# Optimization experiments

Hardware: AMD Instinct MI355X
Metric: run time of the kernel (lower is better)

Reference implementation:

```python
import jax, jax.numpy as jnp
import numpy as np

N_NODES = 50000
N_EDGES = 640000
F_IN = 64
EDGE_DIM = 16
HID = 128
N_LAYERS = 3
N_CLASSES = 2
NUM_GRAPHS = 64
BN_EPS = 1e-5


def setup_inputs() -> dict:
    key = jax.random.key(0)
    ks = jax.random.split(key, 20)
    s = 0.05
    inp = {
        "x": jax.random.normal(ks[0], (N_NODES, F_IN), dtype=jnp.float32),
        "edge_index": jax.random.randint(ks[1], (2, N_EDGES), 0, N_NODES, dtype=jnp.int32),
        "edge_attr": jax.random.normal(ks[2], (N_EDGES, EDGE_DIM), dtype=jnp.float32),
        "batch": jnp.sort(jax.random.randint(ks[3], (N_NODES,), 0, NUM_GRAPHS, dtype=jnp.int32)),
        # node encoder
        "enc_W": jax.random.normal(ks[4], (F_IN, HID), dtype=jnp.float32) * s,
        "enc_b": jnp.zeros((HID,), dtype=jnp.float32),
        # per-layer GINEConv params (stacked over layers)
        "edge_W": jax.random.normal(ks[5], (N_LAYERS, EDGE_DIM, HID), dtype=jnp.float32) * s,
        "edge_b": jnp.zeros((N_LAYERS, HID), dtype=jnp.float32),
        "mlp_W1": jax.random.normal(ks[6], (N_LAYERS, HID, HID), dtype=jnp.float32) * s,
        "mlp_b1": jnp.zeros((N_LAYERS, HID), dtype=jnp.float32),
        "mlp_W2": jax.random.normal(ks[7], (N_LAYERS, HID, HID), dtype=jnp.float32) * s,
        "mlp_b2": jnp.zeros((N_LAYERS, HID), dtype=jnp.float32),
        "bn_gamma": jnp.ones((N_LAYERS, HID), dtype=jnp.float32),
        "bn_beta": jnp.zeros((N_LAYERS, HID), dtype=jnp.float32),
        # classification head
        "head_W1": jax.random.normal(ks[8], (HID, HID), dtype=jnp.float32) * s,
        "head_b1": jnp.zeros((HID,), dtype=jnp.float32),
        "head_W2": jax.random.normal(ks[9], (HID, N_CLASSES), dtype=jnp.float32) * s,
        "head_b2": jnp.zeros((N_CLASSES,), dtype=jnp.float32),
    }
    return inp


def reference(x, edge_index, edge_attr, batch, enc_W, enc_b, edge_W, edge_b,
              mlp_W1, mlp_b1, mlp_W2, mlp_b2, bn_gamma, bn_beta,
              head_W1, head_b1, head_W2, head_b2):
    src, dst = edge_index[0], edge_index[1]  # message flows src -> dst
    h = x @ enc_W + enc_b  # [N, HID]
    for l in range(N_LAYERS):
        # GINEConv: msg = ReLU(x_src + Lin(edge_attr)); aggr = scatter_add at dst
        e = edge_attr @ edge_W[l] + edge_b[l]          # [E, HID]
        msg = jax.nn.relu(h[src] + e)                  # [E, HID]
        agg = jax.ops.segment_sum(msg, dst, num_segments=N_NODES)
        z = h + agg  # (1 + eps) * x + aggr, eps = 0
        # node MLP: Linear-ReLU-Linear
        z = jax.nn.relu(z @ mlp_W1[l] + mlp_b1[l]) @ mlp_W2[l] + mlp_b2[l]
        # BatchNorm1d (training-mode batch stats) + ReLU (dropout = identity)
        mean = jnp.mean(z, axis=0)
        var = jnp.var(z, axis=0)
        z = bn_gamma[l] * (z - mean) * jax.lax.rsqrt(var + BN_EPS) + bn_beta[l]
        h = jax.nn.relu(z)
    # global_add_pool over graphs
    g = jax.ops.segment_sum(h, batch, num_segments=NUM_GRAPHS)  # [G, HID]
    out = jax.nn.relu(g @ head_W1 + head_b1) @ head_W2 + head_b2
    return out  # [G, N_CLASSES]
```

## Files before the change

### kernel.cpp

```cpp
#include <hip/hip_runtime.h>
#include <hip/hip_bf16.h>

#define N_NODES 50000
#define N_EDGES 640000
#define F_IN 64
#define EDGE_DIM 16
#define HID 128
#define N_LAYERS 3
#define NUM_GRAPHS 64
#define BN_EPS 1e-5f

typedef __attribute__((ext_vector_type(8))) short short8;
typedef __attribute__((ext_vector_type(4))) float f32x4;
typedef __attribute__((ext_vector_type(2))) __fp16 half2v;

__device__ __forceinline__ float bfl(unsigned int u) {
    unsigned int v = u << 16; float f; __builtin_memcpy(&f, &v, 4); return f;
}
__device__ __forceinline__ float bfh(unsigned int u) {
    unsigned int v = u & 0xffff0000u; float f; __builtin_memcpy(&f, &v, 4); return f;
}
__device__ __forceinline__ unsigned int f2bf(float f) {
    unsigned int v; __builtin_memcpy(&v, &f, 4);
    v += 0x7fffu + ((v >> 16) & 1u);
    return v >> 16;
}
__device__ __forceinline__ unsigned int pack2(float lo, float hi) {
    return f2bf(lo) | (f2bf(hi) << 16);
}
__device__ __forceinline__ half2v u2h(unsigned int u) {
    half2v h; __builtin_memcpy(&h, &u, 4); return h;
}
__device__ __forceinline__ unsigned int pkh(float a, float b) {
    half2v h = __builtin_amdgcn_cvt_pkrtz(a, b);
    unsigned int u; __builtin_memcpy(&u, &h, 4); return u;
}

__global__ void k_hist(const int* __restrict__ dst, int* __restrict__ deg) {
    int e = blockIdx.x * 256 + threadIdx.x;
    atomicAdd(&deg[dst[e]], 1);
}

__global__ void k_blockred(const int* __restrict__ deg, int* __restrict__ bsums) {
    __shared__ int s[256];
    int i = blockIdx.x * 256 + threadIdx.x;
    int v = (i < N_NODES) ? deg[i] : 0;
    s[threadIdx.x] = v;
    __syncthreads();
    for (int off = 128; off > 0; off >>= 1) {
        if (threadIdx.x < off) s[threadIdx.x] += s[threadIdx.x + off];
        __syncthreads();
    }
    if (threadIdx.x == 0) bsums[blockIdx.x] = s[0];
}

__global__ void k_scan_bsums(int* __restrict__ bsums, int nb) {
    if (threadIdx.x == 0) {
        int run = 0;
        for (int i = 0; i < nb; ++i) { int v = bsums[i]; bsums[i] = run; run += v; }
    }
}

__global__ void k_scan_blocks(int* __restrict__ deg_rowptr, const int* __restrict__ bsums,
                              int* __restrict__ cursor) {
    __shared__ int s[256];
    int tid = threadIdx.x;
    int i = blockIdx.x * 256 + tid;
    int v = (i < N_NODES) ? deg_rowptr[i] : 0;
    s[tid] = v;
    __syncthreads();
    for (int off = 1; off < 256; off <<= 1) {
        int t = 0;
        if (tid >= off) t = s[tid - off];
        __syncthreads();
        s[tid] += t;
        __syncthreads();
    }
    int excl = s[tid] - v + bsums[blockIdx.x];
    if (i < N_NODES) {
        deg_rowptr[i] = excl;
        cursor[i] = excl;
    }
    if (i == N_NODES - 1) deg_rowptr[N_NODES] = N_EDGES;
}

__global__ void k_fill(const int* __restrict__ dst, int* __restrict__ cursor,
                       int* __restrict__ elist) {
    int e = blockIdx.x * 256 + threadIdx.x;
    int p = atomicAdd(&cursor[dst[e]], 1);
    elist[p] = e;
}

__global__ void k_gather(const int* __restrict__ elist, const int* __restrict__ esrc,
                         const float* __restrict__ eattr,
                         int* __restrict__ src_s, uint4* __restrict__ eattr_h) {
    const int p = blockIdx.x * 256 + threadIdx.x;
    const int eid = elist[p];
    src_s[p] = esrc[eid];
    const float4 a0 = *(const float4*)&eattr[eid * EDGE_DIM];
    const float4 a1 = *(const float4*)&eattr[eid * EDGE_DIM + 4];
    const float4 a2 = *(const float4*)&eattr[eid * EDGE_DIM + 8];
    const float4 a3 = *(const float4*)&eattr[eid * EDGE_DIM + 12];
    eattr_h[p * 2] = make_uint4(pkh(a0.x, a0.y), pkh(a0.z, a0.w),
                                pkh(a1.x, a1.y), pkh(a1.z, a1.w));
    eattr_h[p * 2 + 1] = make_uint4(pkh(a2.x, a2.y), pkh(a2.z, a2.w),
                                    pkh(a3.x, a3.y), pkh(a3.z, a3.w));
}

__global__ void k_packW(const float* __restrict__ W1, const float* __restrict__ W2,
                        unsigned short* __restrict__ wp) {
    const int t = blockIdx.x * 256 + threadIdx.x;
    const int mat = t >> 11;
    const int r = t & 2047;
    const int kstep = r >> 9;
    const int ntile = (r >> 6) & 7;
    const int lane = r & 63;
    const float* W = (mat < 3) ? (W1 + mat * 16384) : (W2 + (mat - 3) * 16384);
    const int kbase = kstep * 32 + ((lane >> 4) << 3);
    const int n = ntile * 16 + (lane & 15);
    unsigned int o[4];
#pragma unroll
    for (int jj = 0; jj < 4; ++jj)
        o[jj] = pack2(W[(kbase + 2 * jj) * HID + n], W[(kbase + 2 * jj + 1) * HID + n]);
    *(uint4*)(wp + (size_t)mat * 16384 + (((kstep << 3) + ntile) * 64 + lane) * 8) =
        make_uint4(o[0], o[1], o[2], o[3]);
}

__global__ void k_packEnc(const float* __restrict__ W, unsigned short* __restrict__ wpe) {
    const int t = blockIdx.x * 256 + threadIdx.x;
    const int kstep = t >> 9;
    const int ntile = (t >> 6) & 7;
    const int lane = t & 63;
    const int kbase = kstep * 32 + ((lane >> 4) << 3);
    const int n = ntile * 16 + (lane & 15);
    unsigned int o[4];
#pragma unroll
    for (int jj = 0; jj < 4; ++jj)
        o[jj] = pack2(W[(kbase + 2 * jj) * HID + n], W[(kbase + 2 * jj + 1) * HID + n]);
    *(uint4*)(wpe + (((kstep << 3) + ntile) * 64 + lane) * 8) =
        make_uint4(o[0], o[1], o[2], o[3]);
}

__global__ void k_packWe(const float* __restrict__ eW, unsigned int* __restrict__ wek) {
    const int t = blockIdx.x * 256 + threadIdx.x;
    const int l = t >> 10;
    const int r = t & 1023;
    const int kp = r >> 7, f = r & 127;
    const float a = eW[(l * EDGE_DIM + 2 * kp) * HID + f];
    const float b = eW[(l * EDGE_DIM + 2 * kp + 1) * HID + f];
    wek[t] = pkh(a, b);
}

__global__ void k_xcast(const float* __restrict__ x, unsigned int* __restrict__ xb32) {
    const int i = blockIdx.x * 256 + threadIdx.x;
    const float2 v = *(const float2*)&x[i * 2];
    xb32[i] = pack2(v.x, v.y);
}

__global__ __launch_bounds__(256, 3) void k_encm(const unsigned short* __restrict__ xb,
                                                 const unsigned short* __restrict__ wpe,
                                                 const float* __restrict__ b,
                                                 unsigned short* __restrict__ hb) {
    const int tid = threadIdx.x;
    const int w = tid >> 6, lane = tid & 63;
    const int q = lane >> 4, l15 = lane & 15;
    const int row0 = blockIdx.x * 64 + w * 16;
    const int ar = min(row0 + l15, N_NODES - 1);
    const unsigned short* aptr = xb + (size_t)ar * F_IN + q * 8;
    f32x4 acc[8];
#pragma unroll
    for (int nt = 0; nt < 8; ++nt) acc[nt] = (f32x4){0.f, 0.f, 0.f, 0.f};
#pragma unroll
    for (int ks = 0; ks < 2; ++ks) {
        const short8 a = *(const short8*)(aptr + ks * 32);
#pragma unroll
        for (int nt = 0; nt < 8; ++nt) {
            const short8 bf = *(const short8*)(wpe + (((ks << 3) + nt) * 64 + lane) * 8);
            acc[nt] = __builtin_amdgcn_mfma_f32_16x16x32_bf16(a, bf, acc[nt], 0, 0, 0);
        }
    }
    const int rowb = row0 + q * 4;
#pragma unroll
    for (int nt = 0; nt < 8; ++nt) {
        const float bias = b[nt * 16 + l15];
        const int cc = nt * 16 + l15;
#pragma unroll
        for (int reg = 0; reg < 4; ++reg) {
            const int r = rowb + reg;
            if (r < N_NODES)
                hb[(size_t)r * HID + cc] = (unsigned short)f2bf(acc[nt][reg] + bias);
        }
    }
}

__global__ __launch_bounds__(256, 2) void k_agg(const unsigned int* __restrict__ hb32,
                                                const int* __restrict__ src_s,
                                                const uint4* __restrict__ eattr_h,
                                                const unsigned int* __restrict__ wek,
                                                const float* __restrict__ be,
                                                const int* __restrict__ row_ptr,
                                                unsigned int* __restrict__ zb32) {
    const int lane = threadIdx.x & 63;
    const int wv = threadIdx.x >> 6;
    const int f2 = lane * 2;
    half2v wx[8], wy[8];
#pragma unroll
    for (int j = 0; j < 8; ++j) {
        wx[j] = u2h(wek[j * 128 + f2]);
        wy[j] = u2h(wek[j * 128 + f2 + 1]);
    }
    const float2 eb = *(const float2*)&be[f2];

    const int n = blockIdx.x * 4 + wv;
    const int base = __builtin_amdgcn_readfirstlane(row_ptr[n]);
    const int deg = __builtin_amdgcn_readfirstlane(row_ptr[n + 1]) - base;

    const unsigned int hself = hb32[n * 64 + lane];
    float2 acc = make_float2(bfl(hself), bfh(hself));

    if (deg > 0) {
        const int* sp = src_s + base;
        const uint4* ep = eattr_h + (size_t)base * 2;
        const int last = deg - 1;
        const int nch = (deg + 3) >> 2;

        unsigned int huC[4], huN[4];
        uint4 eaC[4][2], eaN[4][2];
        int s2[4];
        {
            int s0[4], s1[4];
#pragma unroll
            for (int j = 0; j < 4; ++j) s0[j] = sp[min(j, last)];
#pragma unroll
            for (int j = 0; j < 4; ++j) huC[j] = hb32[s0[j] * 64 + lane];
#pragma unroll
            for (int j = 0; j < 4; ++j) s1[j] = sp[min(4 + j, last)];
            if (nch > 1) {
#pragma unroll
                for (int j = 0; j < 4; ++j) huN[j] = hb32[s1[j] * 64 + lane];
            } else {
#pragma unroll
                for (int j = 0; j < 4; ++j) huN[j] = 0u;
            }
#pragma unroll
            for (int j = 0; j < 4; ++j) {
                const int e = min(j, last);
                eaC[j][0] = ep[e * 2]; eaC[j][1] = ep[e * 2 + 1];
            }
#pragma unroll
            for (int j = 0; j < 4; ++j) s2[j] = sp[min(8 + j, last)];
        }
        for (int c = 0; c < nch; ++c) {
            unsigned int huNN[4] = {0u, 0u, 0u, 0u};
            if (c + 2 < nch) {
#pragma unroll
                for (int j = 0; j < 4; ++j) huNN[j] = hb32[s2[j] * 64 + lane];
            }
            int s3[4];
#pragma unroll
            for (int j = 0; j < 4; ++j) s3[j] = sp[min((c + 3) * 4 + j, last)];
            if (c + 1 < nch) {
#pragma unroll
                for (int j = 0; j < 4; ++j) {
                    const int e = min((c + 1) * 4 + j, last);
                    eaN[j][0] = ep[e * 2]; eaN[j][1] = ep[e * 2 + 1];
                }
            }
            const int rem = deg - c * 4;
#pragma unroll
            for (int j = 0; j < 4; ++j) {
                if (j < rem) {
                    const unsigned int* au = (const unsigned int*)&eaC[j][0];
                    float ex = eb.x, ey = eb.y;
#pragma unroll
                    for (int k = 0; k < 8; ++k) {
                        const half2v a = u2h(au[k]);
                        ex = __builtin_amdgcn_fdot2(a, wx[k], ex, false);
                        ey = __builtin_amdgcn_fdot2(a, wy[k], ey, false);
                    }
                    acc.x += fmaxf(bfl(huC[j]) + ex, 0.f);
                    acc.y += fmaxf(bfh(huC[j]) + ey, 0.f);
                }
            }
            if (c + 1 < nch) {
#pragma unroll
                for (int j = 0; j < 4; ++j) {
                    huC[j] = huN[j]; huN[j] = huNN[j];
                    eaC[j][0] = eaN[j][0]; eaC[j][1] = eaN[j][1];
                    s2[j] = s3[j];
                }
            }
        }
    }
    zb32[n * 64 + lane] = pack2(acc.x, acc.y);
}

#define Z1LD 136

__global__ __launch_bounds__(256, 3) void k_mlp(const unsigned short* __restrict__ zb,
                                                const unsigned short* __restrict__ w1p,
                                                const float* __restrict__ b1,
                                                const unsigned short* __restrict__ w2p,
                                                const float* __restrict__ b2,
                                                unsigned short* __restrict__ z2b,
                                                float* __restrict__ bn) {
    __shared__ unsigned short z1s[64 * Z1LD];
    __shared__ float redA[512];
    __shared__ float redB[512];
    const int tid = threadIdx.x;
    const int w = tid >> 6, lane = tid & 63;
    const int q = lane >> 4, l15 = lane & 15;
    const int row0 = blockIdx.x * 64 + w * 16;

    const int ar = min(row0 + l15, N_NODES - 1);
    const unsigned short* aptr = zb + (size_t)ar * HID + q * 8;

    f32x4 acc[8];
#pragma unroll
    for (int nt = 0; nt < 8; ++nt) acc[nt] = (f32x4){0.f, 0.f, 0.f, 0.f};

#pragma unroll
    for (int ks = 0; ks < 4; ++ks) {
        const short8 a = *(const short8*)(aptr + ks * 32);
#pragma unroll
        for (int nt = 0; nt < 8; ++nt) {
            const short8 b = *(const short8*)(w1p + (((ks << 3) + nt) * 64 + lane) * 8);
            acc[nt] = __builtin_amdgcn_mfma_f32_16x16x32_bf16(a, b, acc[nt], 0, 0, 0);
        }
    }
    {
        const int lr0 = w * 16 + q * 4;
#pragma unroll
        for (int nt = 0; nt < 8; ++nt) {
            const float bias = b1[nt * 16 + l15];
            const int cc = nt * 16 + l15;
#pragma unroll
            for (int reg = 0; reg < 4; ++reg) {
                const float v = fmaxf(acc[nt][reg] + bias, 0.f);
                z1s[(lr0 + reg) * Z1LD + cc] = (unsigned short)f2bf(v);
            }
        }
    }
#pragma unroll
    for (int nt = 0; nt < 8; ++nt) acc[nt] = (f32x4){0.f, 0.f, 0.f, 0.f};
    const unsigned short* a2p = &z1s[(w * 16 + l15) * Z1LD + q * 8];
#pragma unroll
    for (int ks = 0; ks < 4; ++ks) {
        const short8 a = *(const short8*)(a2p + ks * 32);
#pragma unroll
        for (int nt = 0; nt < 8; ++nt) {
            const short8 b = *(const short8*)(w2p + (((ks << 3) + nt) * 64 + lane) * 8);
            acc[nt] = __builtin_amdgcn_mfma_f32_16x16x32_bf16(a, b, acc[nt], 0, 0, 0);
        }
    }
    float s[8], sq[8];
    const int rowb = row0 + q * 4;
#pragma unroll
    for (int nt = 0; nt < 8; ++nt) {
        const float bias = b2[nt * 16 + l15];
        const int cc = nt * 16 + l15;
        float ls = 0.f, lq = 0.f;
#pragma unroll
        for (int reg = 0; reg < 4; ++reg) {
            const int r = rowb + reg;
            const float v = acc[nt][reg] + bias;
            if (r < N_NODES) {
                z2b[(size_t)r * HID + cc] = (unsigned short)f2bf(v);
                ls += v;
                lq = fmaf(v, v, lq);
            }
        }
        s[nt] = ls; sq[nt] = lq;
    }
#pragma unroll
    for (int nt = 0; nt < 8; ++nt) {
        s[nt] += __shfl_xor(s[nt], 16, 64);
        s[nt] += __shfl_xor(s[nt], 32, 64);
        sq[nt] += __shfl_xor(sq[nt], 16, 64);
        sq[nt] += __shfl_xor(sq[nt], 32, 64);
    }
    if (lane < 16) {
#pragma unroll
        for (int nt = 0; nt < 8; ++nt) {
            redA[w * 128 + nt * 16 + lane] = s[nt];
            redB[w * 128 + nt * 16 + lane] = sq[nt];
        }
    }
    __syncthreads();
    if (tid < 128) {
        float t = redA[tid] + redA[128 + tid] + redA[256 + tid] + redA[384 + tid];
        atomicAdd(&bn[tid], t);
    } else {
        const int c = tid - 128;
        float t = redB[c] + redB[128 + c] + redB[256 + c] + redB[384 + c];
        atomicAdd(&bn[128 + c], t);
    }
}

__global__ __launch_bounds__(256) void k_bnrelu(const unsigned short* __restrict__ z2b,
                                                const float* __restrict__ bn,
                                                const float* __restrict__ gamma,
                                                const float* __restrict__ beta,
                                                unsigned short* __restrict__ hb) {
    const int idx = (blockIdx.x * 256 + threadIdx.x) * 4;
    const int c = idx & 127;
    const float invN = 1.0f / (float)N_NODES;
    const uint2 zz = *(const uint2*)(z2b + idx);
    float o[4] = {bfl(zz.x), bfh(zz.x), bfl(zz.y), bfh(zz.y)};
#pragma unroll
    for (int k = 0; k < 4; ++k) {
        const float m = bn[c + k] * invN;
        float var = bn[128 + c + k] * invN - m * m;
        var = fmaxf(var, 0.f);
        const float r = rsqrtf(var + BN_EPS);
        o[k] = fmaxf(gamma[c + k] * (o[k] - m) * r + beta[c + k], 0.f);
    }
    *(uint2*)&hb[idx] = make_uint2(pack2(o[0], o[1]), pack2(o[2], o[3]));
}

__global__ void k_pool(const unsigned short* __restrict__ hb, const int* __restrict__ batch,
                       float* __restrict__ g) {
    const int f = threadIdx.x;
    const int n0 = blockIdx.x * 128;
    const int nend = min(n0 + 128, N_NODES);
    float acc = 0.f;
    int cur = batch[n0];
    for (int n = n0; n < nend; ++n) {
        const int bb = batch[n];
        if (bb != cur) {
            atomicAdd(&g[cur * HID + f], acc);
            acc = 0.f;
            cur = bb;
        }
        acc += bfl((unsigned int)hb[n * HID + f]);
    }
    atomicAdd(&g[cur * HID + f], acc);
}

__global__ void k_head1(const float* __restrict__ g, const float* __restrict__ W,
                        const float* __restrict__ b, float* __restrict__ g1) {
    const int idx = blockIdx.x * 256 + threadIdx.x;
    const int r = idx >> 7, c = idx & 127;
    float acc = b[c];
    for (int k = 0; k < 128; ++k) acc = fmaf(g[r * HID + k], W[k * HID + c], acc);
    g1[idx] = fmaxf(acc, 0.f);
}

__global__ void k_head2(const float* __restrict__ g1, const float* __restrict__ W,
                        const float* __restrict__ b, float* __restrict__ out) {
    const int idx = threadIdx.x;
    const int r = idx >> 1, c = idx & 1;
    float acc = b[c];
    for (int k = 0; k < 128; ++k) acc = fmaf(g1[r * HID + k], W[k * 2 + c], acc);
    out[idx] = acc;
}

extern "C" void kernel_launch(void* const* d_in, const int* in_sizes, int n_in,
                              void* d_out, int out_size, void* d_ws, size_t ws_size,
                              hipStream_t stream) {
    const float* x     = (const float*)d_in[0];
    const int*   ei    = (const int*)d_in[1];
    const float* eattr = (const float*)d_in[2];
    const int*   batch = (const int*)d_in[3];
    const float* encW  = (const float*)d_in[4];
    const float* encb  = (const float*)d_in[5];
    const float* eW    = (const float*)d_in[6];
    const float* eb    = (const float*)d_in[7];
    const float* W1    = (const float*)d_in[8];
    const float* b1    = (const float*)d_in[9];
    const float* W2    = (const float*)d_in[10];
    const float* b2    = (const float*)d_in[11];
    const float* gam   = (const float*)d_in[12];
    const float* bet   = (const float*)d_in[13];
    const float* hW1   = (const float*)d_in[14];
    const float* hb1   = (const float*)d_in[15];
    const float* hW2   = (const float*)d_in[16];
    const float* hb2   = (const float*)d_in[17];
    float* out = (float*)d_out;

    float* ws = (float*)d_ws;
    unsigned short* z2b = (unsigned short*)ws;
    float* bn  = ws + 3200000;
    float* g   = ws + 3200256;
    float* g1  = ws + 3208448;
    unsigned short* hb = (unsigned short*)(ws + 3216640);
    unsigned int* zb32 = (unsigned int*)(ws + 6416640);
    unsigned int* xb32 = (unsigned int*)(ws + 9616640);
    int* row_ptr = (int*)(ws + 11216640);
    int* cursor  = row_ptr + N_NODES + 1;
    int* elist   = cursor + N_NODES;
    int* bsums   = elist + N_EDGES;
    int* src_s   = bsums + 256;
    uint4* eattr_h = (uint4*)(ws + 12596900);
    unsigned short* wp  = (unsigned short*)(ws + 17716900);
    unsigned short* wpe = (unsigned short*)(ws + 17766100);
    unsigned int*   wek = (unsigned int*)(ws + 17770200);

    const int* esrc = ei;
    const int* edst = ei + N_EDGES;

    hipMemsetAsync(row_ptr, 0, (N_NODES + 1) * sizeof(int), stream);
    k_hist<<<N_EDGES / 256, 256, 0, stream>>>(edst, row_ptr);
    k_blockred<<<196, 256, 0, stream>>>(row_ptr, bsums);
    k_scan_bsums<<<1, 64, 0, stream>>>(bsums, 196);
    k_scan_blocks<<<196, 256, 0, stream>>>(row_ptr, bsums, cursor);
    k_fill<<<N_EDGES / 256, 256, 0, stream>>>(edst, cursor, elist);
    k_gather<<<N_EDGES / 256, 256, 0, stream>>>(elist, esrc, eattr, src_s, eattr_h);

    k_packW<<<48, 256, 0, stream>>>(W1, W2, wp);
    k_packEnc<<<4, 256, 0, stream>>>(encW, wpe);
    k_packWe<<<12, 256, 0, stream>>>(eW, wek);

    k_xcast<<<6250, 256, 0, stream>>>(x, xb32);
    k_encm<<<782, 256, 0, stream>>>((const unsigned short*)xb32, wpe, encb, hb);

    for (int l = 0; l < N_LAYERS; ++l) {
        k_agg<<<12500, 256, 0, stream>>>((const unsigned int*)hb, src_s, eattr_h,
                                         wek + l * 1024, eb + l * HID, row_ptr, zb32);
        hipMemsetAsync(bn, 0, 256 * sizeof(float), stream);
        k_mlp<<<782, 256, 0, stream>>>((const unsigned short*)zb32,
                                       wp + (size_t)l * 16384, b1 + l * HID,
                                       wp + (size_t)(3 + l) * 16384, b2 + l * HID,
                                       z2b, bn);
        k_bnrelu<<<6250, 256, 0, stream>>>(z2b, bn, gam + l * HID, bet + l * HID, hb);
    }

    hipMemsetAsync(g, 0, NUM_GRAPHS * HID * sizeof(float), stream);
    k_pool<<<391, 128, 0, stream>>>(hb, batch, g);
    k_head1<<<32, 256, 0, stream>>>(g, hW1, hb1, g1);
    k_head2<<<1, 128, 0, stream>>>(g1, hW2, hb2, out);
}
```

Measured before the change: 609.3 us.

## Merge pack kernels, fuse x cast into encoder, persistent aggregation grid

Combines the three weight-packing kernels into one launch and folds the fp32-to-bf16 cast of x into the encoder MFMA kernel, which removes launches and an intermediate buffer round trip. The serial single-thread bsums scan becomes a parallel shared-memory scan. k_gather now handles four edges per thread to expose more memory-level parallelism. k_agg switches to a grid-stride persistent grid of 2048 blocks, so each wave processes many nodes and the weights it loads into registers are reused across them, at some risk of load imbalance across waves.

Result: no change. 608.9 us (-0.1%).

```diff
diff --git a/kernel.cpp b/kernel.cpp
--- a/kernel.cpp
+++ b/kernel.cpp
@@ -9,6 +9,9 @@
 #define N_LAYERS 3
 #define NUM_GRAPHS 64
 #define BN_EPS 1e-5f
+
+#define AGG_BLOCKS 2048
+#define AGG_WAVES (AGG_BLOCKS * 4)
 
 typedef __attribute__((ext_vector_type(8))) short short8;
 typedef __attribute__((ext_vector_type(4))) float f32x4;
@@ -55,10 +58,19 @@
 }
 
 __global__ void k_scan_bsums(int* __restrict__ bsums, int nb) {
-    if (threadIdx.x == 0) {
-        int run = 0;
-        for (int i = 0; i < nb; ++i) { int v = bsums[i]; bsums[i] = run; run += v; }
-    }
+    __shared__ int s[256];
+    const int tid = threadIdx.x;
+    const int v = (tid < nb) ? bsums[tid] : 0;
+    s[tid] = v;
+    __syncthreads();
+    for (int off = 1; off < 256; off <<= 1) {
+        int t = 0;
+        if (tid >= off) t = s[tid - off];
+        __syncthreads();
+        s[tid] += t;
+        __syncthreads();
+    }
+    if (tid < nb) bsums[tid] = s[tid] - v;
 }
 
 __global__ void k_scan_blocks(int* __restrict__ deg_rowptr, const int* __restrict__ bsums,
@@ -91,73 +103,85 @@
     elist[p] = e;
 }
 
-__global__ void k_gather(const int* __restrict__ elist, const int* __restrict__ esrc,
-                         const float* __restrict__ eattr,
-                         int* __restrict__ src_s, uint4* __restrict__ eattr_h) {
-    const int p = blockIdx.x * 256 + threadIdx.x;
-    const int eid = elist[p];
-    src_s[p] = esrc[eid];
-    const float4 a0 = *(const float4*)&eattr[eid * EDGE_DIM];
-    const float4 a1 = *(const float4*)&eattr[eid * EDGE_DIM + 4];
-    const float4 a2 = *(const float4*)&eattr[eid * EDGE_DIM + 8];
-    const float4 a3 = *(const float4*)&eattr[eid * EDGE_DIM + 12];
-    eattr_h[p * 2] = make_uint4(pkh(a0.x, a0.y), pkh(a0.z, a0.w),
-                                pkh(a1.x, a1.y), pkh(a1.z, a1.w));
-    eattr_h[p * 2 + 1] = make_uint4(pkh(a2.x, a2.y), pkh(a2.z, a2.w),
-                                    pkh(a3.x, a3.y), pkh(a3.z, a3.w));
-}
-
-__global__ void k_packW(const float* __restrict__ W1, const float* __restrict__ W2,
-                        unsigned short* __restrict__ wp) {
+__global__ __launch_bounds__(256) void k_gather(const int* __restrict__ elist,
+                                                const int* __restrict__ esrc,
+                                                const float* __restrict__ eattr,
+                                                int* __restrict__ src_s,
+                                                uint4* __restrict__ eattr_h) {
+    const int base = blockIdx.x * 1024;
+    const int tid = threadIdx.x;
+    int p[4], eid[4];
+#pragma unroll
+    for (int j = 0; j < 4; ++j) p[j] = base + tid + j * 256;
+#pragma unroll
+    for (int j = 0; j < 4; ++j) eid[j] = elist[p[j]];
+    int sv[4];
+#pragma unroll
+    for (int j = 0; j < 4; ++j) sv[j] = esrc[eid[j]];
+    float4 a[4][4];
+#pragma unroll
+    for (int j = 0; j < 4; ++j) {
+        const float* ep = eattr + (size_t)eid[j] * EDGE_DIM;
+        a[j][0] = *(const float4*)ep;
+        a[j][1] = *(const float4*)(ep + 4);
+        a[j][2] = *(const float4*)(ep + 8);
+        a[j][3] = *(const float4*)(ep + 12);
+    }
+#pragma unroll
+    for (int j = 0; j < 4; ++j) {
+        src_s[p[j]] = sv[j];
+        eattr_h[p[j] * 2] = make_uint4(pkh(a[j][0].x, a[j][0].y), pkh(a[j][0].z, a[j][0].w),
+                                       pkh(a[j][1].x, a[j][1].y), pkh(a[j][1].z, a[j][1].w));
+        eattr_h[p[j] * 2 + 1] = make_uint4(pkh(a[j][2].x, a[j][2].y), pkh(a[j][2].z, a[j][2].w),
+                                           pkh(a[j][3].x, a[j][3].y), pkh(a[j][3].z, a[j][3].w));
+    }
+}
+
+__global__ void k_pack(const float* __restrict__ W1, const float* __restrict__ W2,
+                       const float* __restrict__ encW, const float* __restrict__ eW,
+                       unsigned short* __restrict__ wp, unsigned short* __restrict__ wpe,
+                       unsigned int* __restrict__ wek) {
     const int t = blockIdx.x * 256 + threadIdx.x;
-    const int mat = t >> 11;
-    const int r = t & 2047;
-    const int kstep = r >> 9;
-    const int ntile = (r >> 6) & 7;
-    const int lane = r & 63;
-    const float* W = (mat < 3) ? (W1 + mat * 16384) : (W2 + (mat - 3) * 16384);
-    const int kbase = kstep * 32 + ((lane >> 4) << 3);
-    const int n = ntile * 16 + (lane & 15);
-    unsigned int o[4];
-#pragma unroll
-    for (int jj = 0; jj < 4; ++jj)
-        o[jj] = pack2(W[(kbase + 2 * jj) * HID + n], W[(kbase + 2 * jj + 1) * HID + n]);
-    *(uint4*)(wp + (size_t)mat * 16384 + (((kstep << 3) + ntile) * 64 + lane) * 8) =
-        make_uint4(o[0], o[1], o[2], o[3]);
-}
-
-__global__ void k_packEnc(const float* __restrict__ W, unsigned short* __restrict__ wpe) {
-    const int t = blockIdx.x * 256 + threadIdx.x;
-    const int kstep = t >> 9;
-    const int ntile = (t >> 6) & 7;
-    const int lane = t & 63;
-    const int kbase = kstep * 32 + ((lane >> 4) << 3);
-    const int n = ntile * 16 + (lane & 15);
-    unsigned int o[4];
-#pragma unroll
-    for (int jj = 0; jj < 4; ++jj)
-        o[jj] = pack2(W[(kbase + 2 * jj) * HID + n], W[(kbase + 2 * jj + 1) * HID + n]);
-    *(uint4*)(wpe + (((kstep << 3) + ntile) * 64 + lane) * 8) =
-        make_uint4(o[0], o[1], o[2], o[3]);
-}
-
-__global__ void k_packWe(const float* __restrict__ eW, unsigned int* __restrict__ wek) {
-    const int t = blockIdx.x * 256 + threadIdx.x;
-    const int l = t >> 10;
-    const int r = t & 1023;
-    const int kp = r >> 7, f = r & 127;
-    const float a = eW[(l * EDGE_DIM + 2 * kp) * HID + f];
-    const float b = eW[(l * EDGE_DIM + 2 * kp + 1) * HID + f];
-    wek[t] = pkh(a, b);
-}
-
-__global__ void k_xcast(const float* __restrict__ x, unsigned int* __restrict__ xb32) {
-    const int i = blockIdx.x * 256 + threadIdx.x;
-    const float2 v = *(const float2*)&x[i * 2];
-    xb32[i] = pack2(v.x, v.y);
-}
-
-__global__ __launch_bounds__(256, 3) void k_encm(const unsigned short* __restrict__ xb,
+    if (t < 12288) {
+        const int mat = t >> 11;
+        const int r = t & 2047;
+        const int kstep = r >> 9;
+        const int ntile = (r >> 6) & 7;
+        const int lane = r & 63;
+        const float* W = (mat < 3) ? (W1 + mat * 16384) : (W2 + (mat - 3) * 16384);
+        const int kbase = kstep * 32 + ((lane >> 4) << 3);
+        const int n = ntile * 16 + (lane & 15);
+        unsigned int o[4];
+#pragma unroll
+        for (int jj = 0; jj < 4; ++jj)
+            o[jj] = pack2(W[(kbase + 2 * jj) * HID + n], W[(kbase + 2 * jj + 1) * HID + n]);
+        *(uint4*)(wp + (size_t)mat * 16384 + (((kstep << 3) + ntile) * 64 + lane) * 8) =
+            make_uint4(o[0], o[1], o[2], o[3]);
+    } else if (t < 13312) {
+        const int r = t - 12288;
+        const int kstep = r >> 9;
+        const int ntile = (r >> 6) & 7;
+        const int lane = r & 63;
+        const int kbase = kstep * 32 + ((lane >> 4) << 3);
+        const int n = ntile * 16 + (lane & 15);
+        unsigned int o[4];
+#pragma unroll
+        for (int jj = 0; jj < 4; ++jj)
+            o[jj] = pack2(encW[(kbase + 2 * jj) * HID + n], encW[(kbase + 2 * jj + 1) * HID + n]);
+        *(uint4*)(wpe + (((kstep << 3) + ntile) * 64 + lane) * 8) =
+            make_uint4(o[0], o[1], o[2], o[3]);
+    } else {
+        const int r = t - 13312;
+        const int l = r >> 10;
+        const int rr = r & 1023;
+        const int kp = rr >> 7, f = rr & 127;
+        const float a = eW[(l * EDGE_DIM + 2 * kp) * HID + f];
+        const float b = eW[(l * EDGE_DIM + 2 * kp + 1) * HID + f];
+        wek[r] = pkh(a, b);
+    }
+}
+
+__global__ __launch_bounds__(256, 3) void k_encm(const float* __restrict__ x,
                                                  const unsigned short* __restrict__ wpe,
                                                  const float* __restrict__ b,
                                                  unsigned short* __restrict__ hb) {
@@ -166,13 +190,17 @@
     const int q = lane >> 4, l15 = lane & 15;
     const int row0 = blockIdx.x * 64 + w * 16;
     const int ar = min(row0 + l15, N_NODES - 1);
-    const unsigned short* aptr = xb + (size_t)ar * F_IN + q * 8;
+    const float* xp = x + (size_t)ar * F_IN + q * 8;
     f32x4 acc[8];
 #pragma unroll
     for (int nt = 0; nt < 8; ++nt) acc[nt] = (f32x4){0.f, 0.f, 0.f, 0.f};
 #pragma unroll
     for (int ks = 0; ks < 2; ++ks) {
-        const short8 a = *(const short8*)(aptr + ks * 32);
+        const float4 v0 = *(const float4*)(xp + ks * 32);
+        const float4 v1 = *(const float4*)(xp + ks * 32 + 4);
+        unsigned int u[4] = {pack2(v0.x, v0.y), pack2(v0.z, v0.w),
+                             pack2(v1.x, v1.y), pack2(v1.z, v1.w)};
+        short8 a; __builtin_memcpy(&a, u, 16);
 #pragma unroll
         for (int nt = 0; nt < 8; ++nt) {
             const short8 bf = *(const short8*)(wpe + (((ks << 3) + nt) * 64 + lane) * 8);
@@ -210,89 +238,91 @@
         wy[j] = u2h(wek[j * 128 + f2 + 1]);
     }
     const float2 eb = *(const float2*)&be[f2];
-
-    const int n = blockIdx.x * 4 + wv;
-    const int base = __builtin_amdgcn_readfirstlane(row_ptr[n]);
-    const int deg = __builtin_amdgcn_readfirstlane(row_ptr[n + 1]) - base;
-
-    const unsigned int hself = hb32[n * 64 + lane];
-    float2 acc = make_float2(bfl(hself), bfh(hself));
-
-    if (deg > 0) {
-        const int* sp = src_s + base;
-        const uint4* ep = eattr_h + (size_t)base * 2;
-        const int last = deg - 1;
-        const int nch = (deg + 3) >> 2;
-
-        unsigned int huC[4], huN[4];
-        uint4 eaC[4][2], eaN[4][2];
-        int s2[4];
-        {
-            int s0[4], s1[4];
-#pragma unroll
-            for (int j = 0; j < 4; ++j) s0[j] = sp[min(j, last)];
-#pragma unroll
-            for (int j = 0; j < 4; ++j) huC[j] = hb32[s0[j] * 64 + lane];
-#pragma unroll
-            for (int j = 0; j < 4; ++j) s1[j] = sp[min(4 + j, last)];
-            if (nch > 1) {
-#pragma unroll
-                for (int j = 0; j < 4; ++j) huN[j] = hb32[s1[j] * 64 + lane];
-            } else {
-#pragma unroll
-                for (int j = 0; j < 4; ++j) huN[j] = 0u;
+    const int wgid = blockIdx.x * 4 + wv;
+
+    for (int n = wgid; n < N_NODES; n += AGG_WAVES) {
+        const int base = __builtin_amdgcn_readfirstlane(row_ptr[n]);
+        const int deg = __builtin_amdgcn_readfirstlane(row_ptr[n + 1]) - base;
+
+        const unsigned int hself = hb32[n * 64 + lane];
+        float2 acc = make_float2(bfl(hself), bfh(hself));
+
+        if (deg > 0) {
+            const int* sp = src_s + base;
+            const uint4* ep = eattr_h + (size_t)base * 2;
+            const int last = deg - 1;
+            const int nch = (deg + 3) >> 2;
+
+            unsigned int huC[4], huN[4];
+            uint4 eaC[4][2], eaN[4][2];
+            int s2[4];
+            {
+                int s0[4], s1[4];
+#pragma unroll
+                for (int j = 0; j < 4; ++j) s0[j] = sp[min(j, last)];
+#pragma unroll
+                for (int j = 0; j < 4; ++j) huC[j] = hb32[s0[j] * 64 + lane];
+#pragma unroll
+                for (int j = 0; j < 4; ++j) s1[j] = sp[min(4 + j, last)];
+                if (nch > 1) {
+#pragma unroll
+                    for (int j = 0; j < 4; ++j) huN[j] = hb32[s1[j] * 64 + lane];
+                } else {
+#pragma unroll
+                    for (int j = 0; j < 4; ++j) huN[j] = 0u;
+                }
+#pragma unroll
+                for (int j = 0; j < 4; ++j) {
+                    const int e = min(j, last);
+                    eaC[j][0] = ep[e * 2]; eaC[j][1] = ep[e * 2 + 1];
+                }
+#pragma unroll
+                for (int j = 0; j < 4; ++j) s2[j] = sp[min(8 + j, last)];
             }
-#pragma unroll
-            for (int j = 0; j < 4; ++j) {
-                const int e = min(j, last);
-                eaC[j][0] = ep[e * 2]; eaC[j][1] = ep[e * 2 + 1];
-            }
-#pragma unroll
-            for (int j = 0; j < 4; ++j) s2[j] = sp[min(8 + j, last)];
-        }
-        for (int c = 0; c < nch; ++c) {
-            unsigned int huNN[4] = {0u, 0u, 0u, 0u};
-            if (c + 2 < nch) {
-#pragma unroll
-                for (int j = 0; j < 4; ++j) huNN[j] = hb32[s2[j] * 64 + lane];
-            }
-            int s3[4];
-#pragma unroll
-            for (int j = 0; j < 4; ++j) s3[j] = sp[min((c + 3) * 4 + j, last)];
-            if (c + 1 < nch) {
+            for (int c = 0; c < nch; ++c) {
+                unsigned int huNN[4] = {0u, 0u, 0u, 0u};
+                if (c + 2 < nch) {
+#pragma unroll
+                    for (int j = 0; j < 4; ++j) huNN[j] = hb32[s2[j] * 64 + lane];
+                }
+                int s3[4];
+#pragma unroll
+                for (int j = 0; j < 4; ++j) s3[j] = sp[min((c + 3) * 4 + j, last)];
+                if (c + 1 < nch) {
+#pragma unroll
+                    for (int j = 0; j < 4; ++j) {
+                        const int e = min((c + 1) * 4 + j, last);
+                        eaN[j][0] = ep[e * 2]; eaN[j][1] = ep[e * 2 + 1];
+                    }
+                }
+                const int rem = deg - c * 4;
 #pragma unroll
                 for (int j = 0; j < 4; ++j) {
-                    const int e = min((c + 1) * 4 + j, last);
-                    eaN[j][0] = ep[e * 2]; eaN[j][1] = ep[e * 2 + 1];
+                    if (j < rem) {
+                        const unsigned int* au = (const unsigned int*)&eaC[j][0];
+                        float ex = eb.x, ey = eb.y;
+#pragma unroll
+                        for (int k = 0; k < 8; ++k) {
+                            const half2v a = u2h(au[k]);
+                            ex = __builtin_amdgcn_fdot2(a, wx[k], ex, false);
+                            ey = __builtin_amdgcn_fdot2(a, wy[k], ey, false);
+                        }
+                        acc.x += fmaxf(bfl(huC[j]) + ex, 0.f);
+                        acc.y += fmaxf(bfh(huC[j]) + ey, 0.f);
+                    }
+                }
+                if (c + 1 < nch) {
+#pragma unroll
+                    for (int j = 0; j < 4; ++j) {
+                        huC[j] = huN[j]; huN[j] = huNN[j];
+                        eaC[j][0] = eaN[j][0]; eaC[j][1] = eaN[j][1];
+                        s2[j] = s3[j];
+                    }
                 }
             }
-            const int rem = deg - c * 4;
-#pragma unroll
-            for (int j = 0; j < 4; ++j) {
-                if (j < rem) {
-                    const unsigned int* au = (const unsigned int*)&eaC[j][0];
-                    float ex = eb.x, ey = eb.y;
-#pragma unroll
-                    for (int k = 0; k < 8; ++k) {
-                        const half2v a = u2h(au[k]);
-                        ex = __builtin_amdgcn_fdot2(a, wx[k], ex, false);
-                        ey = __builtin_amdgcn_fdot2(a, wy[k], ey, false);
-                    }
-                    acc.x += fmaxf(bfl(huC[j]) + ex, 0.f);
-                    acc.y += fmaxf(bfh(huC[j]) + ey, 0.f);
-                }
-            }
-            if (c + 1 < nch) {
-#pragma unroll
-                for (int j = 0; j < 4; ++j) {
-                    huC[j] = huN[j]; huN[j] = huNN[j];
-                    eaC[j][0] = eaN[j][0]; eaC[j][1] = eaN[j][1];
-                    s2[j] = s3[j];
-                }
-            }
-        }
-    }
-    zb32[n * 64 + lane] = pack2(acc.x, acc.y);
+        }
+        zb32[n * 64 + lane] = pack2(acc.x, acc.y);
+    }
 }
 
 #define Z1LD 136
@@ -485,7 +515,6 @@
     float* g1  = ws + 3208448;
     unsigned short* hb = (unsigned short*)(ws + 3216640);
     unsigned int* zb32 = (unsigned int*)(ws + 6416640);
-    unsigned int* xb32 = (unsigned int*)(ws + 9616640);
     int* row_ptr = (int*)(ws + 11216640);
     int* cursor  = row_ptr + N_NODES + 1;
     int* elist   = cursor + N_NODES;
@@ -502,21 +531,18 @@
     hipMemsetAsync(row_ptr, 0, (N_NODES + 1) * sizeof(int), stream);
     k_hist<<<N_EDGES / 256, 256, 0, stream>>>(edst, row_ptr);
     k_blockred<<<196, 256, 0, stream>>>(row_ptr, bsums);
-    k_scan_bsums<<<1, 64, 0, stream>>>(bsums, 196);
+    k_scan_bsums<<<1, 256, 0, stream>>>(bsums, 196);
     k_scan_blocks<<<196, 256, 0, stream>>>(row_ptr, bsums, cursor);
     k_fill<<<N_EDGES / 256, 256, 0, stream>>>(edst, cursor, elist);
-    k_gather<<<N_EDGES / 256, 256, 0, stream>>>(elist, esrc, eattr, src_s, eattr_h);
-
-    k_packW<<<48, 256, 0, stream>>>(W1, W2, wp);
-    k_packEnc<<<4, 256, 0, stream>>>(encW, wpe);
-    k_packWe<<<12, 256, 0, stream>>>(eW, wek);
-
-    k_xcast<<<6250, 256, 0, stream>>>(x, xb32);
-    k_encm<<<782, 256, 0, stream>>>((const unsigned short*)xb32, wpe, encb, hb);
+    k_gather<<<N_EDGES / 1024, 256, 0, stream>>>(elist, esrc, eattr, src_s, eattr_h);
+
+    k_pack<<<64, 256, 0, stream>>>(W1, W2, encW, eW, wp, wpe, wek);
+
+    k_encm<<<782, 256, 0, stream>>>(x, wpe, encb, hb);
 
     for (int l = 0; l < N_LAYERS; ++l) {
-        k_agg<<<12500, 256, 0, stream>>>((const unsigned int*)hb, src_s, eattr_h,
-                                         wek + l * 1024, eb + l * HID, row_ptr, zb32);
+        k_agg<<<AGG_BLOCKS, 256, 0, stream>>>((const unsigned int*)hb, src_s, eattr_h,
+                                              wek + l * 1024, eb + l * HID, row_ptr, zb32);
         hipMemsetAsync(bn, 0, 256 * sizeof(float), stream);
         k_mlp<<<782, 256, 0, stream>>>((const unsigned short*)zb32,
                                        wp + (size_t)l * 16384, b1 + l * HID,
```
